# Kernel optimization log

Hardware: AMD Instinct MI355X
Metric: run time of the kernel (lower is better)

The kernel has to match this reference:

```python
import jax, jax.numpy as jnp
import numpy as np

N = 100000   # num entities / tail rows
D_IN = 128
D_OUT = 128
R = 8        # num relations
E = 131072   # edges per relation
B = 32768    # head entities per relation


def setup_inputs() -> dict:
    key = jax.random.key(0)
    ks = jax.random.split(key, 8)
    x = jax.random.normal(ks[0], (N, D_IN), dtype=jnp.float32)
    tail_rep = jax.random.normal(ks[1], (N, D_IN), dtype=jnp.float32)
    # Linear(in, out, bias=False) weight: [out, in], xavier-ish scale
    W = jax.random.normal(ks[2], (D_OUT, D_IN), dtype=jnp.float32) * (1.414 / np.sqrt(D_IN))
    # match_matrix embedding -> per-relation [in, out] matrices
    rel_W = jax.random.normal(ks[3], (R, D_IN, D_OUT), dtype=jnp.float32) * (1.0 / np.sqrt(D_IN))
    edge_weights = jax.random.uniform(ks[4], (R, E), dtype=jnp.float32)
    edge_rows = jax.random.randint(ks[5], (R, E), 0, B, dtype=jnp.int32)
    edge_cols = jax.random.randint(ks[6], (R, E), 0, N, dtype=jnp.int32)
    # head_indice: unique global entity ids per relation (torch code assigns by index)
    rng = np.random.default_rng(0)
    head = np.stack([rng.choice(N, size=B, replace=False) for _ in range(R)]).astype(np.int32)
    head_indice = jnp.asarray(head)
    return {"x": x, "tail_rep": tail_rep, "W": W, "rel_W": rel_W,
            "edge_weights": edge_weights, "edge_rows": edge_rows,
            "edge_cols": edge_cols, "head_indice": head_indice}


def reference(x, tail_rep, W, rel_W, edge_weights, edge_rows, edge_cols, head_indice):
    # emb_all = original_map(input)
    emb_all = x @ W.T                                   # [N, D_OUT]
    # per-relation dense transform of all tails: tail_rep @ rel_W[r]
    transformed = jnp.einsum('ni,rio->rno', tail_rep, rel_W)   # [R, N, D_OUT]
    # sparse.mm(sp_edge_e, all_rep_h): gather tail rows per edge, weight, segment-sum by local head row
    gathered = jnp.take_along_axis(transformed, edge_cols[:, :, None], axis=1)  # [R, E, D_OUT]
    contrib = edge_weights[:, :, None] * gathered                                # [R, E, D_OUT]
    seg = lambda c, rows: jax.ops.segment_sum(c, rows, num_segments=B)
    new_rep = jax.vmap(seg)(contrib, edge_rows)                                  # [R, B, D_OUT]
    # emb_all[ent_indice] = rel_update + emb_all[ent_indice]  (per relation, sequentially) == scatter-add
    emb_all = emb_all.at[head_indice.reshape(-1)].add(new_rep.reshape(-1, D_OUT))
    # activate=True
    return jax.nn.relu(emb_all)
```

## Files before the change

### kernel.cpp

```cpp
#include <hip/hip_runtime.h>
#include <hip/hip_bf16.h>

#define D_DIM 128
#define N_ENT 100000
#define R_REL 8
#define E_EDGE 131072
#define B_HEAD 32768
#define NH_PAD 100352
#define MAXE (R_REL * E_EDGE)

typedef __attribute__((ext_vector_type(8))) short short8v;
typedef __attribute__((ext_vector_type(16))) float f32x16;
typedef unsigned int uint;
typedef unsigned short ushort;

union BF8 {
  short8v v;
  __hip_bfloat16 h[8];
};

__device__ inline ushort bfbits(float x) {
  union { __hip_bfloat16 h; ushort u; } c;
  c.h = __float2bfloat16(x);
  return c.u;
}
__device__ inline float bflo(uint p) { return __uint_as_float(p << 16); }
__device__ inline float bfhi(uint p) { return __uint_as_float(p & 0xffff0000u); }

__global__ __launch_bounds__(256) void init_ws(int* __restrict__ cnt_e,
                                               int* __restrict__ inv) {
  int i = blockIdx.x * 256 + threadIdx.x;
  if (i < R_REL * B_HEAD) cnt_e[i] = 0;
  inv[i] = -1;
}

__global__ __launch_bounds__(256) void prep_tail(const float* __restrict__ tail,
                                                 short8v* __restrict__ tailb) {
  int i = blockIdx.x * 256 + threadIdx.x;
  const float4* s = (const float4*)tail + (size_t)i * 2;
  float4 a = s[0], b = s[1];
  BF8 h;
  h.h[0] = __float2bfloat16(a.x); h.h[1] = __float2bfloat16(a.y);
  h.h[2] = __float2bfloat16(a.z); h.h[3] = __float2bfloat16(a.w);
  h.h[4] = __float2bfloat16(b.x); h.h[5] = __float2bfloat16(b.y);
  h.h[6] = __float2bfloat16(b.z); h.h[7] = __float2bfloat16(b.w);
  tailb[i] = h.v;
}

__global__ __launch_bounds__(256) void hist_inv(const int* __restrict__ erow,
                                                const int* __restrict__ head,
                                                int* __restrict__ cnt,
                                                int* __restrict__ inv) {
  int bid = blockIdx.x;
  if (bid < 4096) {
    int r = bid >> 9;
    int e = (bid & 511) * 256 + threadIdx.x;
    int row = erow[(size_t)r * E_EDGE + e];
    atomicAdd(cnt + r * B_HEAD + row, 1);
  } else {
    int i = (bid - 4096) * 256 + threadIdx.x;
    int r = i >> 15;
    inv[r * NH_PAD + head[i]] = i & (B_HEAD - 1);
  }
}

__global__ __launch_bounds__(256) void scan_blk(const int* __restrict__ cnt,
                                                int* __restrict__ cur,
                                                int* __restrict__ bsum) {
  int b = blockIdx.x, t = threadIdx.x;
  int4 v = ((const int4*)cnt)[b * 256 + t];
  int s = v.x + v.y + v.z + v.w;
  __shared__ int ps[256];
  ps[t] = s;
  __syncthreads();
  for (int off = 1; off < 256; off <<= 1) {
    int u = (t >= off) ? ps[t - off] : 0;
    __syncthreads();
    ps[t] += u;
    __syncthreads();
  }
  int base = ps[t] - s;
  int4 o;
  o.x = base; o.y = base + v.x; o.z = o.y + v.y; o.w = o.z + v.z;
  ((int4*)cur)[b * 256 + t] = o;
  if (t == 255) bsum[b] = ps[255];
}

__global__ __launch_bounds__(256) void scan_bsum(int* __restrict__ bsum) {
  int t = threadIdx.x;
  int s = bsum[t];
  __shared__ int ps[256];
  ps[t] = s;
  __syncthreads();
  for (int off = 1; off < 256; off <<= 1) {
    int u = (t >= off) ? ps[t - off] : 0;
    __syncthreads();
    ps[t] += u;
    __syncthreads();
  }
  bsum[t] = ps[t] - s;
}

__global__ __launch_bounds__(256) void scatter_edges(const int* __restrict__ erow,
                                                     const int* __restrict__ ecol,
                                                     const float* __restrict__ ew,
                                                     int* __restrict__ cur,
                                                     const int* __restrict__ bsum,
                                                     int2* __restrict__ sColW) {
  int r = blockIdx.y;
  int e = blockIdx.x * 256 + threadIdx.x;
  size_t idx = (size_t)r * E_EDGE + e;
  int row = erow[idx];
  int gi = r * B_HEAD + row;
  int pos = atomicAdd(cur + gi, 1) + bsum[gi >> 10];
  sColW[pos] = make_int2(ecol[idx], __float_as_int(ew[idx]));
}

__global__ __launch_bounds__(256) void prep_W(const float* __restrict__ W,
                                              const float* __restrict__ relW,
                                              short8v* __restrict__ WhS) {
  int mat = blockIdx.y;
  int idx = blockIdx.x * 256 + threadIdx.x;
  int o = idx & 127, ks = idx >> 7;
  float v[8];
  if (mat == 0) {
    const float* src = W + o * D_DIM + ks * 8;
#pragma unroll
    for (int j = 0; j < 8; ++j) v[j] = src[j];
  } else {
    const float* src = relW + (size_t)(mat - 1) * D_DIM * D_DIM + (ks * 8) * D_DIM + o;
#pragma unroll
    for (int j = 0; j < 8; ++j) v[j] = src[j * D_DIM];
  }
  BF8 h;
#pragma unroll
  for (int j = 0; j < 8; ++j) h.h[j] = __float2bfloat16(v[j]);
  WhS[(size_t)mat * 2048 + idx] = h.v;
}

__global__ __launch_bounds__(256) void csr_agg(const uint* __restrict__ tailb,
                                               const int* __restrict__ cur_e,
                                               const int* __restrict__ cnt_e,
                                               const int* __restrict__ bsum,
                                               const int2* __restrict__ sColW,
                                               uint* __restrict__ aggb, int r0) {
  int base = (blockIdx.x << 3) + ((threadIdx.x >> 6) << 1);
  int lane = threadIdx.x & 63;
  int li = lane & 7;
  int f0 = r0 * B_HEAD + base, f1 = f0 + 1;
  int cn0 = cnt_e[f0], cn1 = cnt_e[f1];
  int s0 = cur_e[f0] - cn0 + bsum[f0 >> 10];
  int s1 = cur_e[f1] - cn1 + bsum[f1 >> 10];
  float a0x = 0.f, a0y = 0.f, a1x = 0.f, a1y = 0.f;
  int rounds = ((cn0 > cn1 ? cn0 : cn1) + 7) >> 3;
  for (int rr = 0; rr < rounds; ++rr) {
    int k = rr << 3;
    int i0 = k + li; if (i0 > cn0 - 1) i0 = cn0 > 0 ? cn0 - 1 : 0;
    int i1 = k + li; if (i1 > cn1 - 1) i1 = cn1 > 0 ? cn1 - 1 : 0;
    int g0 = s0 + i0; if (g0 > MAXE - 1) g0 = MAXE - 1;
    int g1 = s1 + i1; if (g1 > MAXE - 1) g1 = MAXE - 1;
    int2 ea = sColW[g0];
    int2 eb = sColW[g1];
#pragma unroll
    for (int j = 0; j < 8; ++j) {
      if (k + j < cn0) {
        int col = __shfl(ea.x, j, 8);
        float w = __int_as_float(__shfl(ea.y, j, 8));
        uint t = tailb[(size_t)col * 64 + lane];
        a0x += w * bflo(t); a0y += w * bfhi(t);
      }
      if (k + j < cn1) {
        int col = __shfl(eb.x, j, 8);
        float w = __int_as_float(__shfl(eb.y, j, 8));
        uint t = tailb[(size_t)col * 64 + lane];
        a1x += w * bflo(t); a1y += w * bfhi(t);
      }
    }
  }
  aggb[(size_t)base * 64 + lane] = (uint)bfbits(a0x) | ((uint)bfbits(a0y) << 16);
  aggb[(size_t)(base + 1) * 64 + lane] = (uint)bfbits(a1x) | ((uint)bfbits(a1y) << 16);
}

__global__ __launch_bounds__(256) void gemm_all(const float* __restrict__ x,
                                                const ushort* __restrict__ aggb,
                                                const short8v* __restrict__ WhS,
                                                float* __restrict__ out,
                                                ushort* __restrict__ updb, int r0,
                                                int nxb) {
  __shared__ short8v wlds[16][128];
  int tid = threadIdx.x;
  int bid = blockIdx.x;
  bool xpart = (bid < nxb);
  int mat, rowbase, relloc = 0;
  if (xpart) {
    mat = 0;
    rowbase = bid * 128;
  } else {
    int b = bid - nxb;
    relloc = b >> 8;
    mat = 1 + r0 + relloc;
    rowbase = (b & 255) * 128;
  }
  const short8v* Bsrc = WhS + (size_t)mat * 2048;
#pragma unroll
  for (int it = 0; it < 8; ++it) {
    int e = it * 256 + tid;
    wlds[e >> 7][e & 127] = Bsrc[e];
  }
  int w = tid >> 6, lane = tid & 63, lrow = lane & 31, lsel = lane >> 5;
  int arow = rowbase + w * 32 + lrow;
  f32x16 acc[4] = {};
  __syncthreads();

  if (xpart) {
    int arowc = (arow < N_ENT) ? arow : (N_ENT - 1);
    const float4* Arow = (const float4*)(x + (size_t)arowc * D_DIM);
#pragma unroll
    for (int kk = 0; kk < 8; ++kk) {
      float4 a0 = Arow[kk * 4 + lsel * 2];
      float4 a1 = Arow[kk * 4 + lsel * 2 + 1];
      BF8 ah;
      ah.h[0] = __float2bfloat16(a0.x); ah.h[1] = __float2bfloat16(a0.y);
      ah.h[2] = __float2bfloat16(a0.z); ah.h[3] = __float2bfloat16(a0.w);
      ah.h[4] = __float2bfloat16(a1.x); ah.h[5] = __float2bfloat16(a1.y);
      ah.h[6] = __float2bfloat16(a1.z); ah.h[7] = __float2bfloat16(a1.w);
      int ks = kk * 2 + lsel;
#pragma unroll
      for (int n = 0; n < 4; ++n)
        acc[n] = __builtin_amdgcn_mfma_f32_32x32x16_bf16(ah.v, wlds[ks][n * 32 + lrow],
                                                         acc[n], 0, 0, 0);
    }
    int wrow0 = rowbase + w * 32;
#pragma unroll
    for (int reg = 0; reg < 16; ++reg) {
      int srow = wrow0 + (reg & 3) + 8 * (reg >> 2) + 4 * lsel;
      if (srow < N_ENT) {
        float* orow = out + (size_t)srow * D_DIM;
#pragma unroll
        for (int n = 0; n < 4; ++n) orow[n * 32 + lrow] = acc[n][reg];
      }
    }
  } else {
    const short8v* Arow =
        (const short8v*)(aggb + ((size_t)relloc * B_HEAD + arow) * D_DIM);
#pragma unroll
    for (int kk = 0; kk < 8; ++kk) {
      short8v a = Arow[kk * 2 + lsel];
      int ks = kk * 2 + lsel;
#pragma unroll
      for (int n = 0; n < 4; ++n)
        acc[n] = __builtin_amdgcn_mfma_f32_32x32x16_bf16(a, wlds[ks][n * 32 + lrow],
                                                         acc[n], 0, 0, 0);
    }
    int wrow0 = rowbase + w * 32;
    ushort* ubase = updb + (size_t)relloc * B_HEAD * D_DIM;
#pragma unroll
    for (int reg = 0; reg < 16; ++reg) {
      int srow = wrow0 + (reg & 3) + 8 * (reg >> 2) + 4 * lsel;
      ushort* urow = ubase + (size_t)srow * D_DIM;
#pragma unroll
      for (int n = 0; n < 4; ++n) urow[n * 32 + lrow] = bfbits(acc[n][reg]);
    }
  }
}

__global__ __launch_bounds__(256) void final_add(const int* __restrict__ inv,
                                                 const ushort* __restrict__ updb,
                                                 float* __restrict__ out, int r0,
                                                 int c, int doRelu) {
  int n = blockIdx.x * 8 + (threadIdx.x >> 5);
  int lane = threadIdx.x & 31;
  if (n >= N_ENT) return;
  float4* o4 = (float4*)out + (size_t)n * 32 + lane;
  float4 v = *o4;
  for (int k = 0; k < c; ++k) {
    int row = inv[(r0 + k) * NH_PAD + n];
    if (row >= 0) {
      uint2 u = ((const uint2*)updb)[((size_t)k * B_HEAD + row) * 32 + lane];
      v.x += bflo(u.x); v.y += bfhi(u.x);
      v.z += bflo(u.y); v.w += bfhi(u.y);
    }
  }
  if (doRelu) {
    v.x = fmaxf(v.x, 0.f); v.y = fmaxf(v.y, 0.f);
    v.z = fmaxf(v.z, 0.f); v.w = fmaxf(v.w, 0.f);
  }
  *o4 = v;
}

extern "C" void kernel_launch(void* const* d_in, const int* in_sizes, int n_in,
                              void* d_out, int out_size, void* d_ws, size_t ws_size,
                              hipStream_t stream) {
  const float* x = (const float*)d_in[0];
  const float* tail = (const float*)d_in[1];
  const float* W = (const float*)d_in[2];
  const float* relW = (const float*)d_in[3];
  const float* ew = (const float*)d_in[4];
  const int* erow = (const int*)d_in[5];
  const int* ecol = (const int*)d_in[6];
  const int* head = (const int*)d_in[7];
  float* out = (float*)d_out;

  char* p = (char*)d_ws;
  short8v* WhS = (short8v*)p;   p += (size_t)(R_REL + 1) * 2048 * 16;
  short8v* tailb = (short8v*)p; p += (size_t)N_ENT * D_DIM * 2;
  int* cnt_e = (int*)p;         p += (size_t)R_REL * B_HEAD * 4;
  int* cur_e = (int*)p;         p += (size_t)R_REL * B_HEAD * 4;
  int* inv = (int*)p;           p += (size_t)R_REL * NH_PAD * 4;
  int* bsum = (int*)p;          p += 256 * 4;
  int2* sColW = (int2*)p;       p += (size_t)R_REL * E_EDGE * 8;
  char* dyn = p;
  size_t fixed = (size_t)(p - (char*)d_ws);
  size_t per_rel = (size_t)B_HEAD * D_DIM * 2 * 2;
  size_t avail = (ws_size > fixed) ? ws_size - fixed : 0;
  int chunk = (int)(avail / per_rel);
  if (chunk > R_REL) chunk = R_REL;
  if (chunk < 1) chunk = 1;
  ushort* aggb = (ushort*)dyn;
  ushort* updb = (ushort*)(dyn + (size_t)chunk * B_HEAD * D_DIM * 2);

  const int NXB = (N_ENT + 127) / 128;

  init_ws<<<dim3(R_REL * NH_PAD / 256), 256, 0, stream>>>(cnt_e, inv);
  prep_W<<<dim3(8, R_REL + 1), 256, 0, stream>>>(W, relW, WhS);
  prep_tail<<<dim3(N_ENT * D_DIM / 8 / 256), 256, 0, stream>>>(tail, tailb);

  hist_inv<<<dim3(4096 + R_REL * B_HEAD / 256), 256, 0, stream>>>(erow, head, cnt_e,
                                                                  inv);
  scan_blk<<<dim3(256), 256, 0, stream>>>(cnt_e, cur_e, bsum);
  scan_bsum<<<dim3(1), 256, 0, stream>>>(bsum);
  scatter_edges<<<dim3(E_EDGE / 256, R_REL), 256, 0, stream>>>(erow, ecol, ew, cur_e,
                                                               bsum, sColW);

  for (int r0 = 0; r0 < R_REL; r0 += chunk) {
    int c = (R_REL - r0 < chunk) ? (R_REL - r0) : chunk;
    csr_agg<<<dim3(c * B_HEAD / 8), 256, 0, stream>>>(
        (const uint*)tailb, cur_e, cnt_e, bsum, sColW, (uint*)aggb, r0);
    int nxb = (r0 == 0) ? NXB : 0;
    gemm_all<<<dim3(nxb + 256 * c), 256, 0, stream>>>(x, aggb, WhS, out, updb, r0,
                                                      nxb);
    final_add<<<dim3((N_ENT + 7) / 8), 256, 0, stream>>>(inv, updb, out, r0, c,
                                                         (r0 + c == R_REL) ? 1 : 0);
  }
}
```

Before: 312.6 us.

## Merge setup kernels and interleave x-GEMM blocks into CSR aggregation launch

Folds the workspace init, weight conversion and tail bf16 conversion into one setup launch. The x@W^T GEMM is moved out of the relation GEMM kernel and interleaved, one block every P, into the CSR aggregation grid. This lets the compute-bound MFMA work overlap with the latency-bound gather work and removes launches. The x-GEMM blocks now read weights straight from global memory instead of LDS, and there are some idle padding blocks.

```diff
diff --git a/kernel.cpp b/kernel.cpp
--- a/kernel.cpp
+++ b/kernel.cpp
@@ -27,24 +27,50 @@
 __device__ inline float bflo(uint p) { return __uint_as_float(p << 16); }
 __device__ inline float bfhi(uint p) { return __uint_as_float(p & 0xffff0000u); }
 
-__global__ __launch_bounds__(256) void init_ws(int* __restrict__ cnt_e,
-                                               int* __restrict__ inv) {
-  int i = blockIdx.x * 256 + threadIdx.x;
-  if (i < R_REL * B_HEAD) cnt_e[i] = 0;
-  inv[i] = -1;
-}
-
-__global__ __launch_bounds__(256) void prep_tail(const float* __restrict__ tail,
-                                                 short8v* __restrict__ tailb) {
-  int i = blockIdx.x * 256 + threadIdx.x;
-  const float4* s = (const float4*)tail + (size_t)i * 2;
-  float4 a = s[0], b = s[1];
-  BF8 h;
-  h.h[0] = __float2bfloat16(a.x); h.h[1] = __float2bfloat16(a.y);
-  h.h[2] = __float2bfloat16(a.z); h.h[3] = __float2bfloat16(a.w);
-  h.h[4] = __float2bfloat16(b.x); h.h[5] = __float2bfloat16(b.y);
-  h.h[6] = __float2bfloat16(b.z); h.h[7] = __float2bfloat16(b.w);
-  tailb[i] = h.v;
+__global__ __launch_bounds__(256) void setup(int* __restrict__ cnt_e,
+                                             int* __restrict__ inv,
+                                             const float* __restrict__ W,
+                                             const float* __restrict__ relW,
+                                             short8v* __restrict__ WhS,
+                                             const float* __restrict__ tail,
+                                             short8v* __restrict__ tailb) {
+  int bid = blockIdx.x;
+  int tid = threadIdx.x;
+  if (bid < 3136) {
+    int i = bid * 256 + tid;
+    if (i < R_REL * B_HEAD) cnt_e[i] = 0;
+    inv[i] = -1;
+  } else if (bid < 3208) {
+    int b = bid - 3136;
+    int mat = b >> 3;
+    int idx = (b & 7) * 256 + tid;
+    int o = idx & 127, ks = idx >> 7;
+    float v[8];
+    if (mat == 0) {
+      const float* src = W + o * D_DIM + ks * 8;
+#pragma unroll
+      for (int j = 0; j < 8; ++j) v[j] = src[j];
+    } else {
+      const float* src =
+          relW + (size_t)(mat - 1) * D_DIM * D_DIM + (ks * 8) * D_DIM + o;
+#pragma unroll
+      for (int j = 0; j < 8; ++j) v[j] = src[j * D_DIM];
+    }
+    BF8 h;
+#pragma unroll
+    for (int j = 0; j < 8; ++j) h.h[j] = __float2bfloat16(v[j]);
+    WhS[(size_t)mat * 2048 + idx] = h.v;
+  } else {
+    int i = (bid - 3208) * 256 + tid;
+    const float4* s = (const float4*)tail + (size_t)i * 2;
+    float4 a = s[0], b = s[1];
+    BF8 h;
+    h.h[0] = __float2bfloat16(a.x); h.h[1] = __float2bfloat16(a.y);
+    h.h[2] = __float2bfloat16(a.z); h.h[3] = __float2bfloat16(a.w);
+    h.h[4] = __float2bfloat16(b.x); h.h[5] = __float2bfloat16(b.y);
+    h.h[6] = __float2bfloat16(b.z); h.h[7] = __float2bfloat16(b.w);
+    tailb[i] = h.v;
+  }
 }
 
 __global__ __launch_bounds__(256) void hist_inv(const int* __restrict__ erow,
@@ -116,36 +142,60 @@
   sColW[pos] = make_int2(ecol[idx], __float_as_int(ew[idx]));
 }
 
-__global__ __launch_bounds__(256) void prep_W(const float* __restrict__ W,
-                                              const float* __restrict__ relW,
-                                              short8v* __restrict__ WhS) {
-  int mat = blockIdx.y;
-  int idx = blockIdx.x * 256 + threadIdx.x;
-  int o = idx & 127, ks = idx >> 7;
-  float v[8];
-  if (mat == 0) {
-    const float* src = W + o * D_DIM + ks * 8;
-#pragma unroll
-    for (int j = 0; j < 8; ++j) v[j] = src[j];
-  } else {
-    const float* src = relW + (size_t)(mat - 1) * D_DIM * D_DIM + (ks * 8) * D_DIM + o;
-#pragma unroll
-    for (int j = 0; j < 8; ++j) v[j] = src[j * D_DIM];
-  }
-  BF8 h;
-#pragma unroll
-  for (int j = 0; j < 8; ++j) h.h[j] = __float2bfloat16(v[j]);
-  WhS[(size_t)mat * 2048 + idx] = h.v;
-}
-
-__global__ __launch_bounds__(256) void csr_agg(const uint* __restrict__ tailb,
-                                               const int* __restrict__ cur_e,
-                                               const int* __restrict__ cnt_e,
-                                               const int* __restrict__ bsum,
-                                               const int2* __restrict__ sColW,
-                                               uint* __restrict__ aggb, int r0) {
-  int base = (blockIdx.x << 3) + ((threadIdx.x >> 6) << 1);
-  int lane = threadIdx.x & 63;
+__global__ __launch_bounds__(256) void fused_csr_xgemm(
+    const uint* __restrict__ tailb, const float* __restrict__ x,
+    const short8v* __restrict__ WhS, const int* __restrict__ cur_e,
+    const int* __restrict__ cnt_e, const int* __restrict__ bsum,
+    const int2* __restrict__ sColW, uint* __restrict__ aggb,
+    float* __restrict__ out, int r0, int nxb, int P, int csrB) {
+  int bid = blockIdx.x;
+  int tid = threadIdx.x;
+  bool isg = (nxb > 0) && (bid % P == 0) && (bid / P < nxb);
+
+  if (isg) {
+    int gid = bid / P;
+    int w = tid >> 6, lane = tid & 63, lrow = lane & 31, lsel = lane >> 5;
+    int rowbase = gid * 128;
+    int arow = rowbase + w * 32 + lrow;
+    int arowc = (arow < N_ENT) ? arow : (N_ENT - 1);
+    const float4* Arow = (const float4*)(x + (size_t)arowc * D_DIM);
+    f32x16 acc[4] = {};
+#pragma unroll
+    for (int kk = 0; kk < 8; ++kk) {
+      int ks = kk * 2 + lsel;
+      short8v b0 = WhS[ks * 128 + 0 * 32 + lrow];
+      short8v b1 = WhS[ks * 128 + 1 * 32 + lrow];
+      short8v b2 = WhS[ks * 128 + 2 * 32 + lrow];
+      short8v b3 = WhS[ks * 128 + 3 * 32 + lrow];
+      float4 a0 = Arow[kk * 4 + lsel * 2];
+      float4 a1 = Arow[kk * 4 + lsel * 2 + 1];
+      BF8 ah;
+      ah.h[0] = __float2bfloat16(a0.x); ah.h[1] = __float2bfloat16(a0.y);
+      ah.h[2] = __float2bfloat16(a0.z); ah.h[3] = __float2bfloat16(a0.w);
+      ah.h[4] = __float2bfloat16(a1.x); ah.h[5] = __float2bfloat16(a1.y);
+      ah.h[6] = __float2bfloat16(a1.z); ah.h[7] = __float2bfloat16(a1.w);
+      acc[0] = __builtin_amdgcn_mfma_f32_32x32x16_bf16(ah.v, b0, acc[0], 0, 0, 0);
+      acc[1] = __builtin_amdgcn_mfma_f32_32x32x16_bf16(ah.v, b1, acc[1], 0, 0, 0);
+      acc[2] = __builtin_amdgcn_mfma_f32_32x32x16_bf16(ah.v, b2, acc[2], 0, 0, 0);
+      acc[3] = __builtin_amdgcn_mfma_f32_32x32x16_bf16(ah.v, b3, acc[3], 0, 0, 0);
+    }
+    int wrow0 = rowbase + w * 32;
+#pragma unroll
+    for (int reg = 0; reg < 16; ++reg) {
+      int srow = wrow0 + (reg & 3) + 8 * (reg >> 2) + 4 * lsel;
+      if (srow < N_ENT) {
+        float* orow = out + (size_t)srow * D_DIM;
+#pragma unroll
+        for (int n = 0; n < 4; ++n) orow[n * 32 + lrow] = acc[n][reg];
+      }
+    }
+    return;
+  }
+
+  int cid = (nxb > 0) ? (bid - bid / P - 1) : bid;
+  if (cid >= csrB) return;
+  int base = (cid << 3) + ((tid >> 6) << 1);
+  int lane = tid & 63;
   int li = lane & 7;
   int f0 = r0 * B_HEAD + base, f1 = f0 + 1;
   int cn0 = cnt_e[f0], cn1 = cnt_e[f1];
@@ -181,26 +231,13 @@
   aggb[(size_t)(base + 1) * 64 + lane] = (uint)bfbits(a1x) | ((uint)bfbits(a1y) << 16);
 }
 
-__global__ __launch_bounds__(256) void gemm_all(const float* __restrict__ x,
-                                                const ushort* __restrict__ aggb,
+__global__ __launch_bounds__(256) void gemm_rel(const ushort* __restrict__ aggb,
                                                 const short8v* __restrict__ WhS,
-                                                float* __restrict__ out,
-                                                ushort* __restrict__ updb, int r0,
-                                                int nxb) {
+                                                ushort* __restrict__ updb, int r0) {
   __shared__ short8v wlds[16][128];
   int tid = threadIdx.x;
-  int bid = blockIdx.x;
-  bool xpart = (bid < nxb);
-  int mat, rowbase, relloc = 0;
-  if (xpart) {
-    mat = 0;
-    rowbase = bid * 128;
-  } else {
-    int b = bid - nxb;
-    relloc = b >> 8;
-    mat = 1 + r0 + relloc;
-    rowbase = (b & 255) * 128;
-  }
+  int relloc = blockIdx.y;
+  int mat = 1 + r0 + relloc;
   const short8v* Bsrc = WhS + (size_t)mat * 2048;
 #pragma unroll
   for (int it = 0; it < 8; ++it) {
@@ -208,59 +245,29 @@
     wlds[e >> 7][e & 127] = Bsrc[e];
   }
   int w = tid >> 6, lane = tid & 63, lrow = lane & 31, lsel = lane >> 5;
+  int rowbase = blockIdx.x * 128;
   int arow = rowbase + w * 32 + lrow;
+  const short8v* Arow =
+      (const short8v*)(aggb + ((size_t)relloc * B_HEAD + arow) * D_DIM);
   f32x16 acc[4] = {};
   __syncthreads();
-
-  if (xpart) {
-    int arowc = (arow < N_ENT) ? arow : (N_ENT - 1);
-    const float4* Arow = (const float4*)(x + (size_t)arowc * D_DIM);
-#pragma unroll
-    for (int kk = 0; kk < 8; ++kk) {
-      float4 a0 = Arow[kk * 4 + lsel * 2];
-      float4 a1 = Arow[kk * 4 + lsel * 2 + 1];
-      BF8 ah;
-      ah.h[0] = __float2bfloat16(a0.x); ah.h[1] = __float2bfloat16(a0.y);
-      ah.h[2] = __float2bfloat16(a0.z); ah.h[3] = __float2bfloat16(a0.w);
-      ah.h[4] = __float2bfloat16(a1.x); ah.h[5] = __float2bfloat16(a1.y);
-      ah.h[6] = __float2bfloat16(a1.z); ah.h[7] = __float2bfloat16(a1.w);
-      int ks = kk * 2 + lsel;
-#pragma unroll
-      for (int n = 0; n < 4; ++n)
-        acc[n] = __builtin_amdgcn_mfma_f32_32x32x16_bf16(ah.v, wlds[ks][n * 32 + lrow],
-                                                         acc[n], 0, 0, 0);
-    }
-    int wrow0 = rowbase + w * 32;
-#pragma unroll
-    for (int reg = 0; reg < 16; ++reg) {
-      int srow = wrow0 + (reg & 3) + 8 * (reg >> 2) + 4 * lsel;
-      if (srow < N_ENT) {
-        float* orow = out + (size_t)srow * D_DIM;
-#pragma unroll
-        for (int n = 0; n < 4; ++n) orow[n * 32 + lrow] = acc[n][reg];
-      }
-    }
-  } else {
-    const short8v* Arow =
-        (const short8v*)(aggb + ((size_t)relloc * B_HEAD + arow) * D_DIM);
-#pragma unroll
-    for (int kk = 0; kk < 8; ++kk) {
-      short8v a = Arow[kk * 2 + lsel];
-      int ks = kk * 2 + lsel;
-#pragma unroll
-      for (int n = 0; n < 4; ++n)
-        acc[n] = __builtin_amdgcn_mfma_f32_32x32x16_bf16(a, wlds[ks][n * 32 + lrow],
-                                                         acc[n], 0, 0, 0);
-    }
-    int wrow0 = rowbase + w * 32;
-    ushort* ubase = updb + (size_t)relloc * B_HEAD * D_DIM;
-#pragma unroll
-    for (int reg = 0; reg < 16; ++reg) {
-      int srow = wrow0 + (reg & 3) + 8 * (reg >> 2) + 4 * lsel;
-      ushort* urow = ubase + (size_t)srow * D_DIM;
-#pragma unroll
-      for (int n = 0; n < 4; ++n) urow[n * 32 + lrow] = bfbits(acc[n][reg]);
-    }
+#pragma unroll
+  for (int kk = 0; kk < 8; ++kk) {
+    short8v a = Arow[kk * 2 + lsel];
+    int ks = kk * 2 + lsel;
+#pragma unroll
+    for (int n = 0; n < 4; ++n)
+      acc[n] = __builtin_amdgcn_mfma_f32_32x32x16_bf16(a, wlds[ks][n * 32 + lrow],
+                                                       acc[n], 0, 0, 0);
+  }
+  int wrow0 = rowbase + w * 32;
+  ushort* ubase = updb + (size_t)relloc * B_HEAD * D_DIM;
+#pragma unroll
+  for (int reg = 0; reg < 16; ++reg) {
+    int srow = wrow0 + (reg & 3) + 8 * (reg >> 2) + 4 * lsel;
+    ushort* urow = ubase + (size_t)srow * D_DIM;
+#pragma unroll
+    for (int n = 0; n < 4; ++n) urow[n * 32 + lrow] = bfbits(acc[n][reg]);
   }
 }
 
@@ -321,10 +328,8 @@
 
   const int NXB = (N_ENT + 127) / 128;
 
-  init_ws<<<dim3(R_REL * NH_PAD / 256), 256, 0, stream>>>(cnt_e, inv);
-  prep_W<<<dim3(8, R_REL + 1), 256, 0, stream>>>(W, relW, WhS);
-  prep_tail<<<dim3(N_ENT * D_DIM / 8 / 256), 256, 0, stream>>>(tail, tailb);
-
+  setup<<<dim3(3136 + 72 + 6250), 256, 0, stream>>>(cnt_e, inv, W, relW, WhS, tail,
+                                                    tailb);
   hist_inv<<<dim3(4096 + R_REL * B_HEAD / 256), 256, 0, stream>>>(erow, head, cnt_e,
                                                                   inv);
   scan_blk<<<dim3(256), 256, 0, stream>>>(cnt_e, cur_e, bsum);
@@ -334,11 +339,17 @@
 
   for (int r0 = 0; r0 < R_REL; r0 += chunk) {
     int c = (R_REL - r0 < chunk) ? (R_REL - r0) : chunk;
-    csr_agg<<<dim3(c * B_HEAD / 8), 256, 0, stream>>>(
-        (const uint*)tailb, cur_e, cnt_e, bsum, sColW, (uint*)aggb, r0);
+    int csrB = c * B_HEAD / 8;
     int nxb = (r0 == 0) ? NXB : 0;
-    gemm_all<<<dim3(nxb + 256 * c), 256, 0, stream>>>(x, aggb, WhS, out, updb, r0,
-                                                      nxb);
+    int P = 1, grid = csrB;
+    if (nxb > 0) {
+      P = (csrB + nxb - 1) / nxb + 1;
+      grid = nxb * P;
+    }
+    fused_csr_xgemm<<<dim3(grid), 256, 0, stream>>>(
+        (const uint*)tailb, x, WhS, cur_e, cnt_e, bsum, sColW, (uint*)aggb, out, r0,
+        nxb, P, csrB);
+    gemm_rel<<<dim3(B_HEAD / 128, c), 256, 0, stream>>>(aggb, WhS, updb, r0);
     final_add<<<dim3((N_ENT + 7) / 8), 256, 0, stream>>>(inv, updb, out, r0, c,
                                                          (r0 + c == R_REL) ? 1 : 0);
   }
```

Result: slower. 428.2 us (+37.0%).
